# Kernel tuning notes

Hardware: AMD Instinct MI355X
Metric: run time of the kernel (lower is better)

The kernel has to match this reference:

```python
import jax, jax.numpy as jnp
import numpy as np

B, C, H, W = 8, 256, 128, 128
WS = 8   # window size
NH = 8   # num heads
NEG = -1e9


def _rel_coords_table(ws):
    # continuous relative coords table, shape [1, 2ws-1, 2ws-1, 2]
    r = np.arange(-(ws - 1), ws, dtype=np.float32)
    t = np.stack(np.meshgrid(r, r, indexing='ij'), axis=-1)[None]
    t = t / (ws - 1) * 8.0
    t = np.sign(t) * np.log2(np.abs(t) + 1.0) / np.log2(8.0)
    return jnp.asarray(t, dtype=jnp.float32)


def _rel_pos_index(ws):
    coords = np.stack(np.meshgrid(np.arange(ws), np.arange(ws), indexing='ij'))  # [2,ws,ws]
    flat = coords.reshape(2, -1)
    rel = (flat[:, :, None] - flat[:, None, :]).transpose(1, 2, 0).astype(np.int64)  # [N,N,2]
    rel[..., 0] += ws - 1
    rel[..., 1] += ws - 1
    rel[..., 0] *= 2 * ws - 1
    return jnp.asarray(rel.sum(-1))  # [N,N]


def setup_inputs() -> dict:
    key = jax.random.key(0)
    ks = jax.random.split(key, 10)
    d8 = C // 8
    return {
        'x': jax.random.normal(ks[0], (B, C, H, W), jnp.float32),
        'y': jax.random.normal(ks[1], (B, C, H, W), jnp.float32),
        'Wq': jax.random.normal(ks[2], (d8, C), jnp.float32) * 0.02,
        'bq': jnp.zeros((d8,), jnp.float32),
        'Wk': jax.random.normal(ks[3], (d8, C), jnp.float32) * 0.02,
        'bk': jnp.zeros((d8,), jnp.float32),
        'Wv': jax.random.normal(ks[4], (C, C), jnp.float32) * 0.02,
        'bv': jnp.zeros((C,), jnp.float32),
        'gamma': jnp.full((1,), 0.5, jnp.float32),
        'qkv_w': jax.random.normal(ks[5], (3 * C, C), jnp.float32) * 0.02,
        'q_bias': jnp.zeros((C,), jnp.float32),
        'v_bias': jnp.zeros((C,), jnp.float32),
        'logit_scale': jnp.log(10.0 * jnp.ones((NH, 1, 1), jnp.float32)),
        'cpb_w1': jax.random.normal(ks[6], (512, 2), jnp.float32) * 0.02,
        'cpb_b1': jnp.zeros((512,), jnp.float32),
        'cpb_w2': jax.random.normal(ks[7], (NH, 512), jnp.float32) * 0.02,
        'proj_w': jax.random.normal(ks[8], (C, C), jnp.float32) * 0.02,
        'proj_b': jnp.zeros((C,), jnp.float32),
    }


def _criss_cross(x, y, Wq, bq, Wk, bk, Wv, bv, gamma):
    # 1x1 convs as einsum channel projections
    q = jnp.einsum('bchw,oc->bohw', x, Wq) + bq[None, :, None, None]
    k = jnp.einsum('bchw,oc->bohw', x, Wk) + bk[None, :, None, None]
    v = jnp.einsum('bchw,oc->bohw', y, Wv) + bv[None, :, None, None]
    h = x.shape[2]
    # column (H-axis) attention with -inf on diagonal; row (W-axis) attention
    diag = jnp.where(jnp.eye(h, dtype=bool), NEG, 0.0).astype(x.dtype)  # [H,H]
    eH = jnp.einsum('bchw,bcgw->bhwg', q, k) + diag[None, :, None, :]   # [B,H,W,H]
    eW = jnp.einsum('bchw,bchv->bhwv', q, k)                            # [B,H,W,W]
    att = jax.nn.softmax(jnp.concatenate([eH, eW], axis=3), axis=3)
    aH, aW = att[..., :h], att[..., h:]
    oH = jnp.einsum('bhwg,bcgw->bchw', aH, v)
    oW = jnp.einsum('bhwv,bchv->bchw', aW, v)
    return gamma[0] * (oH + oW) + x


def _window_attention(xw, qkv_w, q_bias, v_bias, logit_scale,
                      cpb_w1, cpb_b1, cpb_w2, proj_w, proj_b):
    B_, N, Cc = xw.shape
    hd = Cc // NH
    bias = jnp.concatenate([q_bias, jnp.zeros_like(v_bias), v_bias])
    qkv = (xw @ qkv_w.T + bias).reshape(B_, N, 3, NH, hd).transpose(2, 0, 3, 1, 4)
    q, k, v = qkv[0], qkv[1], qkv[2]  # [B_, NH, N, hd]
    qn = q / jnp.maximum(jnp.linalg.norm(q, axis=-1, keepdims=True), 1e-12)
    kn = k / jnp.maximum(jnp.linalg.norm(k, axis=-1, keepdims=True), 1e-12)
    scale = jnp.exp(jnp.minimum(logit_scale, jnp.log(jnp.float32(100.0))))  # [NH,1,1]
    attn = jnp.einsum('bhnd,bhmd->bhnm', qn, kn) * scale[None]
    # continuous relative position bias via inline MLP
    tbl = jax.nn.relu(_rel_coords_table(WS) @ cpb_w1.T + cpb_b1) @ cpb_w2.T  # [1,2ws-1,2ws-1,NH]
    tbl = tbl.reshape(-1, NH)
    rpb = tbl[_rel_pos_index(WS).reshape(-1)].reshape(N, N, NH).transpose(2, 0, 1)
    attn = jax.nn.softmax(attn + (16.0 * jax.nn.sigmoid(rpb))[None], axis=-1)
    out = jnp.einsum('bhnm,bhmd->bnhd', attn, v).reshape(B_, N, Cc)
    return out @ proj_w.T + proj_b


def reference(x, y, Wq, bq, Wk, bk, Wv, bv, gamma,
              qkv_w, q_bias, v_bias, logit_scale,
              cpb_w1, cpb_b1, cpb_w2, proj_w, proj_b):
    cc = _criss_cross(x, y, Wq, bq, Wk, bk, Wv, bv, gamma)   # [B,C,H,W]
    xh = cc.transpose(0, 2, 3, 1)                            # [B,H,W,C]
    win = xh.reshape(B, H // WS, WS, W // WS, WS, C)
    win = win.transpose(0, 1, 3, 2, 4, 5).reshape(-1, WS * WS, C)
    wa = _window_attention(win, qkv_w, q_bias, v_bias, logit_scale,
                           cpb_w1, cpb_b1, cpb_w2, proj_w, proj_b)
    out = wa.reshape(B, H // WS, W // WS, WS, WS, C)
    out = out.transpose(0, 1, 3, 2, 4, 5).reshape(B, H, W, C)
    return out.transpose(0, 3, 1, 2)                         # [B,C,H,W]
```

## Files before the change

kernel.cpp:

```cpp
#include <hip/hip_runtime.h>
#include <cstdio>
#include <cstddef>
#include <cstdint>

#define F_B 8
#define F_C 256
#define F_H 128
#define F_W 128
#define F_HW 16384

typedef __attribute__((ext_vector_type(8))) short short8;
typedef __attribute__((ext_vector_type(4))) short short4v;
typedef __attribute__((ext_vector_type(4))) float float4v;

__device__ __forceinline__ unsigned short f2bf(float f) {
  union {
    float f;
    uint32_t u;
  } v;
  v.f = f;
  return (unsigned short)((v.u + 0x7fffu + ((v.u >> 16) & 1u)) >> 16);
}

__device__ __forceinline__ float bf2f(unsigned short u) {
  union {
    uint32_t u;
    float f;
  } v;
  v.u = ((uint32_t)u) << 16;
  return v.f;
}

__device__ __forceinline__ void async_copy16(const unsigned short* g, unsigned short* l) {
  __builtin_amdgcn_global_load_lds((const __attribute__((address_space(1))) void*)g,
                                   (__attribute__((address_space(3))) void*)l, 16, 0, 0);
}

__global__ void build_aux2(const float* __restrict__ Wq, const float* __restrict__ Wk,
                           const float* __restrict__ bq, const float* __restrict__ bk,
                           const float* __restrict__ q_bias, const float* __restrict__ v_bias,
                           const float* __restrict__ Wv, const float* __restrict__ qkv_w,
                           const float* __restrict__ proj_w, unsigned short* __restrict__ qk_wb,
                           float* __restrict__ qk_b, float* __restrict__ qkv_b,
                           unsigned short* __restrict__ Wvb, unsigned short* __restrict__ qkv_wb,
                           unsigned short* __restrict__ proj_wb) {
  int t = blockIdx.x * 256 + threadIdx.x;
  if (t < 8192) {
    qk_wb[t] = f2bf(Wq[t]);
    qk_wb[8192 + t] = f2bf(Wk[t]);
  }
  if (t < 65536) {
    Wvb[t] = f2bf(Wv[t]);
    proj_wb[t] = f2bf(proj_w[t]);
  }
  if (t < 196608) qkv_wb[t] = f2bf(qkv_w[t]);
  if (t < 32) {
    qk_b[t] = bq[t];
    qk_b[32 + t] = bk[t];
  }
  if (t < 256) {
    qkv_b[t] = q_bias[t];
    qkv_b[256 + t] = 0.0f;
    qkv_b[512 + t] = v_bias[t];
  }
}

__device__ __forceinline__ float cpb_coord(int a) {
  float v = (float)(a - 7) * (8.0f / 7.0f);
  float lg = log2f(fabsf(v) + 1.0f) * (1.0f / 3.0f);
  return (v < 0.0f) ? -lg : lg;
}

__global__ void cpb_table(const float* __restrict__ w1, const float* __restrict__ b1,
                          const float* __restrict__ w2, float* __restrict__ tblS) {
  int e = blockIdx.x;
  int yi = e / 15, xi = e % 15;
  float ry = cpb_coord(yi), rx = cpb_coord(xi);
  __shared__ float hid[512];
  int t = threadIdx.x;
  for (int j = t; j < 512; j += 256) {
    float hv = w1[j * 2] * ry + w1[j * 2 + 1] * rx + b1[j];
    hid[j] = fmaxf(hv, 0.0f);
  }
  __syncthreads();
  if (t < 8) {
    float s = 0.0f;
    for (int j = 0; j < 512; j++) s += hid[j] * w2[t * 512 + j];
    tblS[e * 8 + t] = 16.0f / (1.0f + __expf(-s));
  }
}

__global__ void build_rpbt(const float* __restrict__ tblS, float* __restrict__ rpbt) {
  int t = blockIdx.x * 256 + threadIdx.x;
  int h = t >> 12, i = (t >> 6) & 63, j = t & 63;
  int e = ((i >> 3) - (j >> 3) + 7) * 15 + ((i & 7) - (j & 7) + 7);
  rpbt[t] = tblS[e * 8 + h];
}

__global__ void transpose_bf(const float* __restrict__ in, unsigned short* __restrict__ outb) {
  __shared__ float tile[32][33];
  int b = blockIdx.z;
  int p0 = blockIdx.x * 32;
  int c0 = blockIdx.y * 32;
  const float* src = in + (size_t)b * F_C * F_HW;
  int tx = threadIdx.x, ty = threadIdx.y;
#pragma unroll
  for (int i = 0; i < 4; i++) {
    tile[ty + i * 8][tx] = src[(size_t)(c0 + ty + i * 8) * F_HW + p0 + tx];
  }
  __syncthreads();
#pragma unroll
  for (int i = 0; i < 4; i++) {
    size_t idx = (size_t)b * F_HW * F_C + (size_t)(p0 + ty + i * 8) * F_C + c0 + tx;
    outb[idx] = f2bf(tile[tx][ty + i * 8]);
  }
}

template <int BN, int OUT>
__global__ __launch_bounds__(256) void gemm_mfma(const unsigned short* __restrict__ A,
                                                 const unsigned short* __restrict__ Wt,
                                                 const float* __restrict__ bias, void* Cmat,
                                                 int M, int N, int gx) {
  constexpr int WN = BN / 2;
  constexpr int NREP = WN / 16;
  __shared__ __align__(16) unsigned short As[128 * 32];
  __shared__ __align__(16) unsigned short Bs[BN * 32];
  int nwg = gridDim.x;
  int id = blockIdx.x;
  int cpx = nwg >> 3;
  int swz = (id & 7) * cpx + (id >> 3);
  int by = swz / gx;
  int bx = swz - by * gx;
  int m0 = by * 128;
  int n0 = bx * BN;
  int t = threadIdx.x;
  int wid = t >> 6, lane = t & 63;
  int wr = wid >> 1, wc = wid & 1;

  float4v acc[4][NREP] = {};

  for (int k0 = 0; k0 < 256; k0 += 32) {
    __syncthreads();
#pragma unroll
    for (int j = 0; j < 2; j++) {
      int r = wid * 32 + j * 16 + (lane >> 2);
      int kg = (lane & 3) ^ ((r >> 1) & 3);
      const unsigned short* gp = A + (size_t)(m0 + r) * 256 + k0 + kg * 8;
      async_copy16(gp, As + (wid * 32 + j * 16) * 32);
    }
#pragma unroll
    for (int j = 0; j < BN / 64; j++) {
      int r = wid * (BN / 4) + j * 16 + (lane >> 2);
      int kg = (lane & 3) ^ ((r >> 1) & 3);
      const unsigned short* gp = Wt + (size_t)(n0 + r) * 256 + k0 + kg * 8;
      async_copy16(gp, Bs + (wid * (BN / 4) + j * 16) * 32);
    }
    __syncthreads();
    short8 af[4];
#pragma unroll
    for (int mi = 0; mi < 4; mi++) {
      int row = wr * 64 + mi * 16 + (lane & 15);
      int kg = (lane >> 4) ^ ((row >> 1) & 3);
      af[mi] = *(const short8*)(As + row * 32 + kg * 8);
    }
    short8 bfr[NREP];
#pragma unroll
    for (int ni = 0; ni < NREP; ni++) {
      int col = wc * WN + ni * 16 + (lane & 15);
      int kg = (lane >> 4) ^ ((col >> 1) & 3);
      bfr[ni] = *(const short8*)(Bs + col * 32 + kg * 8);
    }
#pragma unroll
    for (int mi = 0; mi < 4; mi++)
#pragma unroll
      for (int ni = 0; ni < NREP; ni++)
        acc[mi][ni] =
            __builtin_amdgcn_mfma_f32_16x16x32_bf16(af[mi], bfr[ni], acc[mi][ni], 0, 0, 0);
  }
#pragma unroll
  for (int ni = 0; ni < NREP; ni++) {
    int col = n0 + wc * WN + ni * 16 + (lane & 15);
    float bn = bias[col];
#pragma unroll
    for (int mi = 0; mi < 4; mi++) {
      int row0 = m0 + wr * 64 + mi * 16 + (lane >> 4) * 4;
#pragma unroll
      for (int r = 0; r < 4; r++) {
        float v = acc[mi][ni][r] + bn;
        int row = row0 + r;
        if (OUT == 0) {
          ((float*)Cmat)[(size_t)row * N + col] = v;
        } else if (OUT == 1) {
          int bb = row >> 14, p = row & 16383;
          ((float*)Cmat)[((size_t)bb * N + col) * F_HW + p] = v;
        } else {
          ((unsigned short*)Cmat)[(size_t)row * N + col] = f2bf(v);
        }
      }
    }
  }
}

template <int MODE>
__global__ __launch_bounds__(256) void cc_logits(const float* __restrict__ qk,
                                                 unsigned short* __restrict__ e,
                                                 float* __restrict__ sums) {
  int x = blockIdx.x;
  int b = blockIdx.y;
  size_t base = (size_t)b * F_HW;
  __shared__ float kt[32][132];
  int t = threadIdx.x;
  {
    int gk = t >> 1, c0 = (t & 1) * 16;
    size_t krow = (MODE == 0) ? ((size_t)gk * F_W + x) : ((size_t)x * F_W + gk);
    const float4* src = (const float4*)(qk + (base + krow) * 64 + 32 + c0);
#pragma unroll
    for (int q4 = 0; q4 < 4; q4++) {
      float4 v = src[q4];
      kt[c0 + q4 * 4 + 0][gk] = v.x;
      kt[c0 + q4 * 4 + 1][gk] = v.y;
      kt[c0 + q4 * 4 + 2][gk] = v.z;
      kt[c0 + q4 * 4 + 3][gk] = v.w;
    }
  }
  __syncthreads();
  int i = t >> 1, g0 = (t & 1) * 64;
  size_t qrow = (MODE == 0) ? ((size_t)i * F_W + x) : ((size_t)x * F_W + i);
  const float4* qp = (const float4*)(qk + (base + qrow) * 64);
  float qreg[32];
#pragma unroll
  for (int q4 = 0; q4 < 8; q4++) {
    float4 v = qp[q4];
    qreg[q4 * 4 + 0] = v.x;
    qreg[q4 * 4 + 1] = v.y;
    qreg[q4 * 4 + 2] = v.z;
    qreg[q4 * 4 + 3] = v.w;
  }
  float acc[64];
#pragma unroll
  for (int g = 0; g < 64; g++) acc[g] = 0.0f;
  for (int c = 0; c < 32; c++) {
    float qv = qreg[c];
#pragma unroll
    for (int g = 0; g < 64; g++) acc[g] += qv * kt[c][g0 + g];
  }
  if (MODE == 0) {
    int d = i - g0;
    if (d >= 0 && d < 64) acc[d] = -1e9f;
  }
  unsigned short* ep = e + (base + qrow) * 256 + MODE * 128 + g0;
  float s = 0.0f;
#pragma unroll
  for (int g = 0; g < 64; g += 8) {
    short8 pk;
#pragma unroll
    for (int j = 0; j < 8; j++) {
      float ev = __expf(acc[g + j]);
      s += ev;
      pk[j] = (short)f2bf(ev);
    }
    *(short8*)(ep + g) = pk;
  }
  s += __shfl_xor(s, 1);
  if ((t & 1) == 0) sums[base + qrow] = s;
}

template <int MODE>
__global__ __launch_bounds__(256) void cc_pv_mfma(const unsigned short* __restrict__ eb,
                                                  const unsigned short* __restrict__ vtb,
                                                  const float* __restrict__ sumH,
                                                  const float* __restrict__ sumW,
                                                  const float* __restrict__ gamma,
                                                  const unsigned short* __restrict__ xb,
                                                  unsigned short* __restrict__ pob,
                                                  unsigned short* __restrict__ ccb) {
  int x = blockIdx.x, b = blockIdx.y;
  size_t base = (size_t)b * F_HW;
  __shared__ __align__(16) unsigned short As[128 * 128];
  __shared__ __align__(16) unsigned short Vs[256 * 64];
  int t = threadIdx.x;
  int wid = t >> 6, lane = t & 63;
  int wr = wid >> 1, wc = wid & 1;
  {
    int i = t >> 1, half = t & 1;
    size_t pix = (MODE == 0) ? ((size_t)i * F_W + x) : ((size_t)x * F_W + i);
    float rv = 1.0f / (sumH[base + pix] + sumW[base + pix]);
    const unsigned short* ep = eb + (base + pix) * 256 + MODE * 128 + half * 64;
    int g = ((i >> 3) & 7) ^ (i & 7);
#pragma unroll
    for (int s = 0; s < 8; s++) {
      short8 vin = *(const short8*)(ep + s * 8);
      short8 vo;
#pragma unroll
      for (int j = 0; j < 8; j++) vo[j] = (short)f2bf(bf2f((unsigned short)vin[j]) * rv);
      int slot = (half * 8 + s) ^ g;
      *(short8*)(As + i * 128 + slot * 8) = vo;
    }
  }
  float4v acc[4][8] = {};
#pragma unroll
  for (int kc = 0; kc < 2; kc++) {
    __syncthreads();
    {
      int ko = t >> 5, cj = t & 31;
      short8 rowv[8];
#pragma unroll
      for (int r = 0; r < 8; r++) {
        int kk = kc * 64 + ko * 8 + r;
        size_t pixk = (MODE == 0) ? ((size_t)kk * F_W + x) : ((size_t)x * F_W + kk);
        rowv[r] = *(const short8*)(vtb + (base + pixk) * 256 + cj * 8);
      }
#pragma unroll
      for (int j = 0; j < 8; j++) {
        short8 col;
#pragma unroll
        for (int r = 0; r < 8; r++) col[r] = rowv[r][j];
        int c = cj * 8 + j;
        int slot = ko ^ ((c >> 3) & 7) ^ (c & 7);
        *(short8*)(Vs + c * 64 + slot * 8) = col;
      }
    }
    __syncthreads();
#pragma unroll
    for (int ksub = 0; ksub < 2; ksub++) {
      short8 af[4];
#pragma unroll
      for (int mi = 0; mi < 4; mi++) {
        int i = wr * 64 + mi * 16 + (lane & 15);
        int slot = (kc * 8 + ksub * 4 + (lane >> 4)) ^ ((i >> 3) & 7) ^ (i & 7);
        af[mi] = *(const short8*)(As + i * 128 + slot * 8);
      }
      short8 bfv[8];
#pragma unroll
      for (int ni = 0; ni < 8; ni++) {
        int c = wc * 128 + ni * 16 + (lane & 15);
        int slot = (ksub * 4 + (lane >> 4)) ^ ((c >> 3) & 7) ^ (c & 7);
        bfv[ni] = *(const short8*)(Vs + c * 64 + slot * 8);
      }
#pragma unroll
      for (int mi = 0; mi < 4; mi++)
#pragma unroll
        for (int ni = 0; ni < 8; ni++)
          acc[mi][ni] =
              __builtin_amdgcn_mfma_f32_16x16x32_bf16(af[mi], bfv[ni], acc[mi][ni], 0, 0, 0);
    }
  }
  float gm = gamma[0];
#pragma unroll
  for (int mi = 0; mi < 4; mi++) {
#pragma unroll
    for (int ni = 0; ni < 8; ni++) {
#pragma unroll
      for (int r = 0; r < 4; r++) {
        int i = wr * 64 + mi * 16 + (lane >> 4) * 4 + r;
        int c = wc * 128 + ni * 16 + (lane & 15);
        size_t pix = (MODE == 0) ? ((size_t)i * F_W + x) : ((size_t)x * F_W + i);
        size_t idx = (base + pix) * 256 + c;
        if (MODE == 0) {
          pob[idx] = f2bf(acc[mi][ni][r]);
        } else {
          float v = gm * (bf2f(pob[idx]) + acc[mi][ni][r]) + bf2f(xb[idx]);
          ccb[idx] = f2bf(v);
        }
      }
    }
  }
}

__global__ __launch_bounds__(512, 2) void win_fused(
    const unsigned short* __restrict__ ccb, const unsigned short* __restrict__ qkv_wb,
    const float* __restrict__ qkv_b, const float* __restrict__ logit_scale,
    const float* __restrict__ rpbt, unsigned short* __restrict__ out) {
  __shared__ __align__(16) unsigned short As[64 * 256];
  __shared__ __align__(16) unsigned short Bs[2][128 * 32];
  __shared__ __align__(16) unsigned short QKV[3 * 64 * 256];
  int tid = threadIdx.x;
  int wid = tid >> 6, lane = tid & 63;
  int il = lane & 15, kg = lane >> 4;
  int win = blockIdx.x;
  int b = win >> 8, wy = (win >> 4) & 15, wx = win & 15;
  size_t pbase = (size_t)b * F_HW + (size_t)(wy * 8) * F_W + wx * 8;

#pragma unroll
  for (int i = 0; i < 4; i++) {
    int n = i * 16 + (tid >> 5);
    int slot = tid & 31;
    size_t srow = pbase + (size_t)(n >> 3) * F_W + (n & 7);
    async_copy16(ccb + srow * 256 + (size_t)(slot ^ (n & 7)) * 8, As + n * 256 + slot * 8);
  }

  int rB = tid >> 2, ksB = tid & 3;
  int kgB = ksB ^ ((rB >> 1) & 3);
  for (int nc = 0; nc < 6; nc++) {
    int col0 = nc * 128;
    const unsigned short* wp = qkv_wb + (size_t)(col0 + rB) * 256 + kgB * 8;
    async_copy16(wp, Bs[0] + rB * 32 + ksB * 8);
    __syncthreads();
    float4v acc[4] = {};
    int cur = 0;
    for (int k0 = 0; k0 < 256; k0 += 32) {
      if (k0 < 224) async_copy16(wp + k0 + 32, Bs[cur ^ 1] + rB * 32 + ksB * 8);
      int colW = wid * 16 + il;
      short8 bfr = *(const short8*)(Bs[cur] + colW * 32 + (kg ^ ((colW >> 1) & 3)) * 8);
#pragma unroll
      for (int mi = 0; mi < 4; mi++) {
        int row = mi * 16 + il;
        int slot = ((k0 >> 3) + kg) ^ (row & 7);
        short8 af = *(const short8*)(As + row * 256 + slot * 8);
        acc[mi] = __builtin_amdgcn_mfma_f32_16x16x32_bf16(af, bfr, acc[mi], 0, 0, 0);
      }
      __syncthreads();
      cur ^= 1;
    }
    int cg = col0 + wid * 16 + il;
    int sec = cg >> 8, cs = cg & 255;
    float bn = qkv_b[cg];
    unsigned short* qp = QKV + sec * 16384;
#pragma unroll
    for (int mi = 0; mi < 4; mi++) {
#pragma unroll
      for (int r = 0; r < 4; r++) {
        int n = mi * 16 + kg * 4 + r;
        qp[n * 256 + (((cs >> 3) ^ (n & 7)) * 8) + (cs & 7)] = f2bf(acc[mi][r] + bn);
      }
    }
  }
  __syncthreads();

  int hh = wid;
  unsigned short* Pl_w = QKV + wid * 4096;
  unsigned short* Vt_w = As + wid * 2048;

  short8 qb[4], ka[4];
#pragma unroll
  for (int ni = 0; ni < 4; ni++) {
    int i = ni * 16 + il;
    int so = ((hh * 4 + kg) ^ (i & 7)) * 8;
    short8 qv = *(const short8*)(QKV + i * 256 + so);
    short8 kv = *(const short8*)(QKV + 16384 + i * 256 + so);
    float qss = 0.0f, kss = 0.0f;
#pragma unroll
    for (int j = 0; j < 8; j++) {
      float qf = bf2f((unsigned short)qv[j]);
      float kf = bf2f((unsigned short)kv[j]);
      qss += qf * qf;
      kss += kf * kf;
    }
    qss += __shfl_xor(qss, 16);
    qss += __shfl_xor(qss, 32);
    kss += __shfl_xor(kss, 16);
    kss += __shfl_xor(kss, 32);
    float qinv = 1.0f / fmaxf(sqrtf(qss), 1e-12f);
    float kinv = 1.0f / fmaxf(sqrtf(kss), 1e-12f);
#pragma unroll
    for (int j = 0; j < 8; j++) {
      qb[ni][j] = (short)f2bf(bf2f((unsigned short)qv[j]) * qinv);
      ka[ni][j] = (short)f2bf(bf2f((unsigned short)kv[j]) * kinv);
    }
  }

  if (lane < 32) {
    int jb = lane >> 2, db = lane & 3;
    short8 rows[8];
#pragma unroll
    for (int r = 0; r < 8; r++) {
      rows[r] = *(const short8*)(QKV + 32768 + (jb * 8 + r) * 256 + (((hh * 4 + db) ^ r) * 8));
    }
#pragma unroll
    for (int c = 0; c < 8; c++) {
      int d = db * 8 + c;
      short8 col;
#pragma unroll
      for (int r = 0; r < 8; r++) col[r] = rows[r][c];
      *(short8*)(Vt_w + d * 64 + ((jb ^ (d & 7)) * 8)) = col;
    }
  }

  float4v sacc[4][4] = {};
#pragma unroll
  for (int mj = 0; mj < 4; mj++)
#pragma unroll
    for (int ni = 0; ni < 4; ni++)
      sacc[mj][ni] =
          __builtin_amdgcn_mfma_f32_16x16x32_bf16(ka[mj], qb[ni], sacc[mj][ni], 0, 0, 0);

  float scale = __expf(fminf(logit_scale[hh], 4.605170185988091f));
  __syncthreads();

#pragma unroll
  for (int ni = 0; ni < 4; ni++) {
    int i = ni * 16 + il;
    const float* rp = rpbt + ((size_t)hh * 64 + i) * 64;
    float sv[16];
    float mx = -1e30f;
#pragma unroll
    for (int mj = 0; mj < 4; mj++) {
      float4 rb = *(const float4*)(rp + mj * 16 + kg * 4);
      float rbs[4] = {rb.x, rb.y, rb.z, rb.w};
#pragma unroll
      for (int r = 0; r < 4; r++) {
        float v = sacc[mj][ni][r] * scale + rbs[r];
        sv[mj * 4 + r] = v;
        mx = fmaxf(mx, v);
      }
    }
    mx = fmaxf(mx, __shfl_xor(mx, 16));
    mx = fmaxf(mx, __shfl_xor(mx, 32));
    float sm = 0.0f;
#pragma unroll
    for (int u = 0; u < 16; u++) {
      sv[u] = __expf(sv[u] - mx);
      sm += sv[u];
    }
    sm += __shfl_xor(sm, 16);
    sm += __shfl_xor(sm, 32);
    float inv = 1.0f / sm;
#pragma unroll
    for (int mj = 0; mj < 4; mj++) {
      int j0 = mj * 16 + kg * 4;
      short4v pk;
#pragma unroll
      for (int r = 0; r < 4; r++) pk[r] = (short)f2bf(sv[mj * 4 + r] * inv);
      int byteoff = i * 128 + (((j0 >> 3) ^ (i & 7)) * 16) + (j0 & 7) * 2;
      *(short4v*)((char*)Pl_w + byteoff) = pk;
    }
  }
  __syncthreads();

  float4v oacc[2][4] = {};
#pragma unroll
  for (int kc = 0; kc < 2; kc++) {
    short8 va[2];
#pragma unroll
    for (int md = 0; md < 2; md++) {
      int d = md * 16 + il;
      va[md] = *(const short8*)((char*)Vt_w + d * 128 + (((kc * 4 + kg) ^ (d & 7)) * 16));
    }
    short8 pb[4];
#pragma unroll
    for (int ni = 0; ni < 4; ni++) {
      int i = ni * 16 + il;
      pb[ni] = *(const short8*)((char*)Pl_w + i * 128 + (((kc * 4 + kg) ^ (i & 7)) * 16));
    }
#pragma unroll
    for (int md = 0; md < 2; md++)
#pragma unroll
      for (int ni = 0; ni < 4; ni++)
        oacc[md][ni] =
            __builtin_amdgcn_mfma_f32_16x16x32_bf16(va[md], pb[ni], oacc[md][ni], 0, 0, 0);
  }

#pragma unroll
  for (int ni = 0; ni < 4; ni++) {
    int i = ni * 16 + il;
    size_t orow = (pbase + (size_t)(i >> 3) * F_W + (i & 7)) * 256 + hh * 32;
#pragma unroll
    for (int md = 0; md < 2; md++) {
      int d0 = md * 16 + kg * 4;
      short4v pk;
#pragma unroll
      for (int r = 0; r < 4; r++) pk[r] = (short)f2bf(oacc[md][ni][r]);
      *(short4v*)(out + orow + d0) = pk;
    }
  }
}

extern "C" void kernel_launch(void* const* d_in, const int* in_sizes, int n_in,
                              void* d_out, int out_size, void* d_ws, size_t ws_size,
                              hipStream_t stream) {
  const float* x = (const float*)d_in[0];
  const float* y = (const float*)d_in[1];
  const float* Wq = (const float*)d_in[2];
  const float* bq = (const float*)d_in[3];
  const float* Wk = (const float*)d_in[4];
  const float* bk = (const float*)d_in[5];
  const float* Wv = (const float*)d_in[6];
  const float* bv = (const float*)d_in[7];
  const float* gamma = (const float*)d_in[8];
  const float* qkv_w = (const float*)d_in[9];
  const float* q_bias = (const float*)d_in[10];
  const float* v_bias = (const float*)d_in[11];
  const float* logit_scale = (const float*)d_in[12];
  const float* cpb_w1 = (const float*)d_in[13];
  const float* cpb_b1 = (const float*)d_in[14];
  const float* cpb_w2 = (const float*)d_in[15];
  const float* proj_w = (const float*)d_in[16];
  const float* proj_b = (const float*)d_in[17];

  float* ws = (float*)d_ws;
  const size_t NPX = (size_t)F_B * F_HW;
  const size_t M1 = NPX * 256;
  size_t f_xb = 0;
  size_t f_ytb = M1 / 2;
  size_t f_vtb = M1;
  size_t f_pob = M1 + M1 / 2;
  size_t f_ccb = 2 * M1;
  size_t f_qkb = 2 * M1 + M1 / 2;
  size_t f_wts = f_qkb + NPX * 64;
  size_t o_qkwb = f_wts;
  size_t o_Wvb = o_qkwb + 8192;
  size_t o_qkvwb = o_Wvb + 32768;
  size_t o_projwb = o_qkvwb + 98304;
  size_t o_qkb2 = o_projwb + 32768;
  size_t o_qkvb2 = o_qkb2 + 64;
  size_t o_tbl = o_qkvb2 + 768;
  size_t o_sumH = o_tbl + 1800;
  size_t o_sumW = o_sumH + NPX;
  size_t o_rpbt = o_sumW + NPX;
  size_t need = (o_rpbt + 32768) * sizeof(float);
  if (ws_size < need) {
    fprintf(stderr, "kernel_launch: ws too small: %zu < %zu\n", ws_size, need);
    return;
  }
  unsigned short* xb = (unsigned short*)(ws + f_xb);
  unsigned short* ytb = (unsigned short*)(ws + f_ytb);
  unsigned short* eb = (unsigned short*)(ws + f_ytb);
  unsigned short* vtb = (unsigned short*)(ws + f_vtb);
  unsigned short* pob = (unsigned short*)(ws + f_pob);
  unsigned short* attn_b = (unsigned short*)(ws + f_pob);
  unsigned short* ccb = (unsigned short*)(ws + f_ccb);
  float* qkb = ws + f_qkb;
  unsigned short* qk_wb = (unsigned short*)(ws + o_qkwb);
  unsigned short* Wvb = (unsigned short*)(ws + o_Wvb);
  unsigned short* qkv_wb = (unsigned short*)(ws + o_qkvwb);
  unsigned short* proj_wb = (unsigned short*)(ws + o_projwb);
  float* qk_b = ws + o_qkb2;
  float* qkv_b = ws + o_qkvb2;
  float* tblS = ws + o_tbl;
  float* sumH = ws + o_sumH;
  float* sumW = ws + o_sumW;
  float* rpbt = ws + o_rpbt;

  build_aux2<<<dim3(768), dim3(256), 0, stream>>>(Wq, Wk, bq, bk, q_bias, v_bias, Wv, qkv_w,
                                                  proj_w, qk_wb, qk_b, qkv_b, Wvb, qkv_wb,
                                                  proj_wb);
  cpb_table<<<dim3(225), dim3(256), 0, stream>>>(cpb_w1, cpb_b1, cpb_w2, tblS);
  build_rpbt<<<dim3(128), dim3(256), 0, stream>>>(tblS, rpbt);
  transpose_bf<<<dim3(512, 8, 8), dim3(32, 8), 0, stream>>>(x, xb);
  transpose_bf<<<dim3(512, 8, 8), dim3(32, 8), 0, stream>>>(y, ytb);
  gemm_mfma<64, 0><<<dim3(1024), dim3(256), 0, stream>>>(xb, qk_wb, qk_b, qkb, (int)NPX, 64,
                                                         1);
  gemm_mfma<128, 2><<<dim3(2048), dim3(256), 0, stream>>>(ytb, Wvb, bv, vtb, (int)NPX, 256, 2);
  cc_logits<0><<<dim3(128, 8), dim3(256), 0, stream>>>(qkb, eb, sumH);
  cc_logits<1><<<dim3(128, 8), dim3(256), 0, stream>>>(qkb, eb, sumW);
  cc_pv_mfma<0><<<dim3(128, 8), dim3(256), 0, stream>>>(eb, vtb, sumH, sumW, gamma, xb, pob,
                                                        ccb);
  cc_pv_mfma<1><<<dim3(128, 8), dim3(256), 0, stream>>>(eb, vtb, sumH, sumW, gamma, xb, pob,
                                                        ccb);
  win_fused<<<dim3(2048), dim3(512), 0, stream>>>(ccb, qkv_wb, qkv_b, logit_scale, rpbt,
                                                  attn_b);
  gemm_mfma<128, 1><<<dim3(2048), dim3(256), 0, stream>>>(attn_b, proj_wb, proj_b, d_out,
                                                          (int)NPX, 256, 2);
}
```

Measured before the change: 609.8 us.

## Give each wave a private weight buffer and drop block barriers in the QKV GEMM

Each wave now double-buffers its own 16-column slice of the QKV weight in shared memory, so the per-k-step block-wide __syncthreads calls are removed. The MFMA operands are swapped so the accumulator layout lets each lane write four contiguous bf16 outputs as one vector store, and the bias is read as a float4. A-fragments are loaded before the next async copy is issued, and the MFMA burst runs at raised wave priority. The risk is correctness: with no barrier, the async copy into each wave's buffer depends on wait semantics that are not visible here.

```diff
diff --git a/kernel.cpp b/kernel.cpp
--- a/kernel.cpp
+++ b/kernel.cpp
@@ -372,7 +372,7 @@
     const float* __restrict__ qkv_b, const float* __restrict__ logit_scale,
     const float* __restrict__ rpbt, unsigned short* __restrict__ out) {
   __shared__ __align__(16) unsigned short As[64 * 256];
-  __shared__ __align__(16) unsigned short Bs[2][128 * 32];
+  __shared__ __align__(16) unsigned short Bs[8][2][512];
   __shared__ __align__(16) unsigned short QKV[3 * 64 * 256];
   int tid = threadIdx.x;
   int wid = tid >> 6, lane = tid & 63;
@@ -388,41 +388,46 @@
     size_t srow = pbase + (size_t)(n >> 3) * F_W + (n & 7);
     async_copy16(ccb + srow * 256 + (size_t)(slot ^ (n & 7)) * 8, As + n * 256 + slot * 8);
   }
-
-  int rB = tid >> 2, ksB = tid & 3;
-  int kgB = ksB ^ ((rB >> 1) & 3);
+  __syncthreads();
+
+  int r16 = lane >> 2, ks = lane & 3;
+  int kgB = ks ^ ((r16 >> 1) & 3);
+  unsigned short* Bw = &Bs[wid][0][0];
   for (int nc = 0; nc < 6; nc++) {
     int col0 = nc * 128;
-    const unsigned short* wp = qkv_wb + (size_t)(col0 + rB) * 256 + kgB * 8;
-    async_copy16(wp, Bs[0] + rB * 32 + ksB * 8);
-    __syncthreads();
+    const unsigned short* wp = qkv_wb + (size_t)(col0 + wid * 16 + r16) * 256 + kgB * 8;
+    async_copy16(wp, Bw + lane * 8);
     float4v acc[4] = {};
     int cur = 0;
     for (int k0 = 0; k0 < 256; k0 += 32) {
-      if (k0 < 224) async_copy16(wp + k0 + 32, Bs[cur ^ 1] + rB * 32 + ksB * 8);
-      int colW = wid * 16 + il;
-      short8 bfr = *(const short8*)(Bs[cur] + colW * 32 + (kg ^ ((colW >> 1) & 3)) * 8);
+      short8 bfr = *(const short8*)(Bw + cur * 512 + il * 32 + (kg ^ ((il >> 1) & 3)) * 8);
+      short8 af[4];
 #pragma unroll
       for (int mi = 0; mi < 4; mi++) {
         int row = mi * 16 + il;
         int slot = ((k0 >> 3) + kg) ^ (row & 7);
-        short8 af = *(const short8*)(As + row * 256 + slot * 8);
-        acc[mi] = __builtin_amdgcn_mfma_f32_16x16x32_bf16(af, bfr, acc[mi], 0, 0, 0);
-      }
-      __syncthreads();
+        af[mi] = *(const short8*)(As + row * 256 + slot * 8);
+      }
+      if (k0 < 224) async_copy16(wp + k0 + 32, Bw + (cur ^ 1) * 512 + lane * 8);
+      __builtin_amdgcn_s_setprio(1);
+#pragma unroll
+      for (int mi = 0; mi < 4; mi++)
+        acc[mi] = __builtin_amdgcn_mfma_f32_16x16x32_bf16(bfr, af[mi], acc[mi], 0, 0, 0);
+      __builtin_amdgcn_s_setprio(0);
       cur ^= 1;
     }
-    int cg = col0 + wid * 16 + il;
+    int cg = col0 + wid * 16 + kg * 4;
     int sec = cg >> 8, cs = cg & 255;
-    float bn = qkv_b[cg];
+    float4 bn4 = *(const float4*)(qkv_b + cg);
+    float bns[4] = {bn4.x, bn4.y, bn4.z, bn4.w};
     unsigned short* qp = QKV + sec * 16384;
 #pragma unroll
     for (int mi = 0; mi < 4; mi++) {
-#pragma unroll
-      for (int r = 0; r < 4; r++) {
-        int n = mi * 16 + kg * 4 + r;
-        qp[n * 256 + (((cs >> 3) ^ (n & 7)) * 8) + (cs & 7)] = f2bf(acc[mi][r] + bn);
-      }
+      int n = mi * 16 + il;
+      short4v pk;
+#pragma unroll
+      for (int r = 0; r < 4; r++) pk[r] = (short)f2bf(acc[mi][r] + bns[r]);
+      *(short4v*)(qp + n * 256 + (((cs >> 3) ^ (n & 7)) * 8) + (cs & 7)) = pk;
     }
   }
   __syncthreads();
```

Result: faster. 584.2 us (-4.2%).
